# Kernel optimization log

Hardware: AMD Instinct MI355X
Metric: run time of the kernel (lower is better)

Reference implementation:

```python
import jax, jax.numpy as jnp
import numpy as np

N, OBS_LEN, PRED_LEN = 8192, 20, 30
EMBED, HIDDEN, CNN_OUT = 64, 128, 2048


def setup_inputs() -> dict:
    key = jax.random.key(0)
    ks = jax.random.split(key, 13)
    s = 0.05
    return {
        "img_embedding": jax.random.normal(ks[0], (N, CNN_OUT), jnp.float32),
        "obs_pos": jax.random.normal(ks[1], (N, OBS_LEN, 2), jnp.float32),
        "obs_hist_size": jax.random.randint(ks[2], (N,), 0, 20, jnp.int64) if jax.config.jax_enable_x64 else jax.random.randint(ks[2], (N,), 0, 20, jnp.int32),
        "obs_pos_rel": jax.random.normal(ks[3], (N, OBS_LEN, 2), jnp.float32),
        "h0": jax.random.normal(ks[4], (1, HIDDEN), jnp.float32) * s,
        "W_ih": jax.random.normal(ks[5], (4 * HIDDEN, EMBED), jnp.float32) * s,
        "W_hh": jax.random.normal(ks[6], (4 * HIDDEN, HIDDEN), jnp.float32) * s,
        "b_ih": jax.random.normal(ks[7], (4 * HIDDEN,), jnp.float32) * s,
        "b_hh": jax.random.normal(ks[8], (4 * HIDDEN,), jnp.float32) * s,
        "embed_W": jax.random.normal(ks[9], (EMBED, 2), jnp.float32) * s,
        "embed_b": jax.random.normal(ks[10], (EMBED,), jnp.float32) * s,
        "pred_W": jax.random.normal(ks[11], (2, HIDDEN + CNN_OUT), jnp.float32) * s,
        "pred_b": jax.random.normal(ks[12], (2,), jnp.float32) * s,
    }


def reference(img_embedding, obs_pos, obs_hist_size, obs_pos_rel,
              h0, W_ih, W_hh, b_ih, b_hh, embed_W, embed_b, pred_W, pred_b):
    n, obs_len = obs_pos.shape[0], obs_pos.shape[1]

    def lstm_cell(x_emb, h, c):
        # torch gate order: i, f, g, o
        gates = x_emb @ W_ih.T + b_ih + h @ W_hh.T + b_hh  # [n, 4H]
        i, f, g, o = jnp.split(gates, 4, axis=-1)
        c2 = jax.nn.sigmoid(f) * c + jax.nn.sigmoid(i) * jnp.tanh(g)
        h2 = jax.nn.sigmoid(o) * jnp.tanh(c2)
        return h2, c2

    def embed(rel):
        return jax.nn.relu(rel @ embed_W.T + embed_b)

    # NOTE: original code initializes BOTH h and c from h0 (faithful to source).
    h = jnp.broadcast_to(h0, (n, h0.shape[1]))
    c = h

    # ---- observation phase: t = 1 .. obs_len-1, masked update ----
    def obs_step(carry, inp):
        h, c = carry
        rel_t, t = inp
        mask = (obs_hist_size > (obs_len - t))[:, None]  # [n, 1]
        h2, c2 = lstm_cell(embed(rel_t), h, c)
        h = jnp.where(mask, h2, h)
        c = jnp.where(mask, c2, c)
        return (h, c), None

    ts = jnp.arange(1, obs_len)
    rel_seq = jnp.swapaxes(obs_pos_rel[:, 1:, :], 0, 1)  # [obs_len-1, n, 2]
    (h, c), _ = jax.lax.scan(obs_step, (h, c), (rel_seq, ts))

    def pred_step(carry, _):
        h, c, pos = carry
        disp = jnp.concatenate([h, img_embedding], axis=1) @ pred_W.T + pred_b  # [n, 2]
        pos = pos + disp
        h, c = lstm_cell(embed(disp), h, c)
        return (h, c, pos), pos

    pos0 = obs_pos[:, -1, :]
    _, traj = jax.lax.scan(pred_step, (h, c, pos0), None, length=PRED_LEN)
    return jnp.swapaxes(traj, 0, 1)  # [n, pred_len, 2]
```

## Files before the change

### kernel.cpp

```cpp
#include <hip/hip_runtime.h>

#define MBLK 32

typedef __attribute__((ext_vector_type(8))) short bf16x8;
typedef __attribute__((ext_vector_type(4))) short bf16x4;
typedef __attribute__((ext_vector_type(4))) float f32x4;

__device__ __forceinline__ unsigned short f2bf(float x){
  unsigned int u = __float_as_uint(x);
  u = u + 0x7FFFu + ((u >> 16) & 1u);
  return (unsigned short)(u >> 16);
}
__device__ __forceinline__ float bf2f(unsigned short s){
  return __uint_as_float(((unsigned int)s) << 16);
}
__device__ __forceinline__ float sigm(float x){
  return __builtin_amdgcn_rcpf(1.0f + __expf(-x));
}
__device__ __forceinline__ float tanh_(float x){
  return 1.0f - 2.0f*__builtin_amdgcn_rcpf(__expf(2.0f*x) + 1.0f);
}

__global__ __launch_bounds__(1024, 4) void traj_kernel(
    const float* __restrict__ img, const float* __restrict__ obs_pos,
    const int* __restrict__ hist, const float* __restrict__ rel,
    const float* __restrict__ h0, const float* __restrict__ W_ih,
    const float* __restrict__ W_hh, const float* __restrict__ b_ih,
    const float* __restrict__ b_hh, const float* __restrict__ eW,
    const float* __restrict__ eb, const float* __restrict__ pW,
    const float* __restrict__ pb, float* __restrict__ out)
{
  __shared__ unsigned short xh[2][MBLK*200];
  __shared__ float relL[MBLK*40];
  __shared__ float pwL[256];
  __shared__ float eW0[64], eW1[64], ebL[64];
  __shared__ float imgcL[MBLK*2];
  __shared__ float biasL[512];
  __shared__ float pbL[2];

  const int tid  = threadIdx.x;
  const int wv   = tid >> 6;
  const int lane = tid & 63;
  const int q    = lane >> 4;
  const int i    = lane & 15;
  const int par  = i & 1;
  const int j    = wv*8 + (i >> 1);
  const int g0   = blockIdx.x * MBLK;
  const int dm   = tid >> 5;
  const int i32  = tid & 31;

  for (int idx = tid; idx < MBLK*40; idx += 1024) relL[idx] = rel[g0*40 + idx];
  if (tid < 256) pwL[tid] = pW[(tid >> 7)*2176 + (tid & 127)];
  if (tid < 64){ eW0[tid] = eW[tid*2]; eW1[tid] = eW[tid*2+1]; ebL[tid] = eb[tid]; }
  if (tid < 512) biasL[tid] = b_ih[tid] + b_hh[tid];
  if (tid < 2) pbL[tid] = pb[tid];

  {
    const float* row = img + (size_t)(g0 + dm)*2048 + i32*64;
    const float* p0  = pW + 128 + i32*64;
    const float* p1  = pW + 2176 + 128 + i32*64;
    float s0 = 0.f, s1 = 0.f;
    #pragma unroll
    for (int v = 0; v < 16; v++){
      float4 a  = ((const float4*)row)[v];
      float4 w0 = ((const float4*)p0)[v];
      float4 w1 = ((const float4*)p1)[v];
      s0 += a.x*w0.x + a.y*w0.y + a.z*w0.z + a.w*w0.w;
      s1 += a.x*w1.x + a.y*w1.y + a.z*w1.z + a.w*w1.w;
    }
    #pragma unroll
    for (int msk = 1; msk < 32; msk <<= 1){
      s0 += __shfl_xor(s0, msk);
      s1 += __shfl_xor(s1, msk);
    }
    if (i32 == 0){ imgcL[dm*2] = s0; imgcL[dm*2+1] = s1; }
  }

  float h0j = h0[j];
  unsigned int thrpk = 0;
  float c_s[4];
  #pragma unroll
  for (int r = 0; r < 4; r++){
    int m = par*16 + q*4 + r;
    thrpk |= ((unsigned int)((20 - hist[g0 + m]) & 0xFF)) << (8*r);
    c_s[r] = h0j;
    xh[0][m*200 + 64 + j] = f2bf(h0j);
  }

  bf16x8 Bf[2][6];
  #pragma unroll
  for (int n2 = 0; n2 < 2; n2++){
    int row = (n2*2 + par)*128 + j;
    #pragma unroll
    for (int kt = 0; kt < 6; kt++){
      const float* src = (kt < 2) ? (W_ih + row*64  + kt*32      + q*8)
                                  : (W_hh + row*128 + (kt-2)*32  + q*8);
      float4 lo = ((const float4*)src)[0];
      float4 hi = ((const float4*)src)[1];
      bf16x8 tf;
      tf[0]=(short)f2bf(lo.x); tf[1]=(short)f2bf(lo.y); tf[2]=(short)f2bf(lo.z); tf[3]=(short)f2bf(lo.w);
      tf[4]=(short)f2bf(hi.x); tf[5]=(short)f2bf(hi.y); tf[6]=(short)f2bf(hi.z); tf[7]=(short)f2bf(hi.w);
      Bf[n2][kt] = tf;
    }
  }

  float pos_r = 0.f;
  if (i32 < 2) pos_r = obs_pos[(size_t)(g0 + dm)*40 + 38 + i32];

  __syncthreads();

  {
    int e0 = i32*2;
    float r0 = relL[dm*40 + 2], r1 = relL[dm*40 + 3];
    float a0 = fmaxf(0.f, r0*eW0[e0]   + r1*eW1[e0]   + ebL[e0]);
    float a1 = fmaxf(0.f, r0*eW0[e0+1] + r1*eW1[e0+1] + ebL[e0+1]);
    *((unsigned int*)&xh[0][dm*200 + e0]) =
        (unsigned int)f2bf(a0) | ((unsigned int)f2bf(a1) << 16);
  }

  int b = 0;

  for (int step = 0; step < 49; step++){
    const bool obs = (step < 19);
    __syncthreads();

    if (!obs){
      bf16x4 hv = *((const bf16x4*)&xh[b][dm*200 + 64 + i32*4]);
      float s0 = 0.f, s1 = 0.f;
      #pragma unroll
      for (int u = 0; u < 4; u++){
        float hf = bf2f((unsigned short)hv[u]);
        s0 += hf * pwL[i32*4 + u];
        s1 += hf * pwL[128 + i32*4 + u];
      }
      s0 += __shfl_xor(s0, 1);  s1 += __shfl_xor(s1, 1);
      s0 += __shfl_xor(s0, 2);  s1 += __shfl_xor(s1, 2);
      s0 += __shfl_xor(s0, 4);  s1 += __shfl_xor(s1, 4);
      s0 += __shfl_xor(s0, 8);  s1 += __shfl_xor(s1, 8);
      s0 += __shfl_xor(s0, 16); s1 += __shfl_xor(s1, 16);
      float d0 = s0 + imgcL[dm*2]   + pbL[0];
      float d1 = s1 + imgcL[dm*2+1] + pbL[1];
      if (i32 < 2){
        pos_r += (i32 == 0) ? d0 : d1;
        out[(size_t)(g0 + dm)*60 + (size_t)(step - 19)*2 + i32] = pos_r;
      }
      int e0 = i32*2;
      float a0 = fmaxf(0.f, d0*eW0[e0]   + d1*eW1[e0]   + ebL[e0]);
      float a1 = fmaxf(0.f, d0*eW0[e0+1] + d1*eW1[e0+1] + ebL[e0+1]);
      *((unsigned int*)&xh[b][dm*200 + e0]) =
          (unsigned int)f2bf(a0) | ((unsigned int)f2bf(a1) << 16);
      __syncthreads();
    }

    const float bv0 = biasL[(par    )*128 + j];
    const float bv1 = biasL[(2 + par)*128 + j];
    f32x4 a00 = (f32x4){bv0, bv0, bv0, bv0};
    f32x4 a01 = (f32x4){bv1, bv1, bv1, bv1};
    f32x4 a10 = a00;
    f32x4 a11 = a01;
    {
      bf16x8 A[6];
      #pragma unroll
      for (int kt = 0; kt < 6; kt++)
        A[kt] = *((const bf16x8*)&xh[b][i*200 + kt*32 + q*8]);
      #pragma unroll
      for (int kt = 0; kt < 6; kt++){
        a00 = __builtin_amdgcn_mfma_f32_16x16x32_bf16(A[kt], Bf[0][kt], a00, 0, 0, 0);
        a01 = __builtin_amdgcn_mfma_f32_16x16x32_bf16(A[kt], Bf[1][kt], a01, 0, 0, 0);
      }
    }
    {
      bf16x8 A[6];
      #pragma unroll
      for (int kt = 0; kt < 6; kt++)
        A[kt] = *((const bf16x8*)&xh[b][(16 + i)*200 + kt*32 + q*8]);
      #pragma unroll
      for (int kt = 0; kt < 6; kt++){
        a10 = __builtin_amdgcn_mfma_f32_16x16x32_bf16(A[kt], Bf[0][kt], a10, 0, 0, 0);
        a11 = __builtin_amdgcn_mfma_f32_16x16x32_bf16(A[kt], Bf[1][kt], a11, 0, 0, 0);
      }
    }

    if (obs && step < 18){
      int tt = step + 2;
      int e0 = i32*2;
      float r0 = relL[dm*40 + tt*2], r1 = relL[dm*40 + tt*2 + 1];
      float a0 = fmaxf(0.f, r0*eW0[e0]   + r1*eW1[e0]   + ebL[e0]);
      float a1 = fmaxf(0.f, r0*eW0[e0+1] + r1*eW1[e0+1] + ebL[e0+1]);
      *((unsigned int*)&xh[b^1][dm*200 + e0]) =
          (unsigned int)f2bf(a0) | ((unsigned int)f2bf(a1) << 16);
    }

    f32x4 self0 = par ? a10 : a00;
    f32x4 self1 = par ? a11 : a01;
    f32x4 send0 = par ? a00 : a10;
    f32x4 send1 = par ? a01 : a11;

    #pragma unroll
    for (int r = 0; r < 4; r++){
      float y0 = __shfl_xor(send0[r], 1);
      float y1 = __shfl_xor(send1[r], 1);
      float a0 = self0[r];
      float a1 = self1[r];
      float ig = par ? y0 : a0;
      float fg = par ? a0 : y0;
      float gg = par ? y1 : a1;
      float og = par ? a1 : y1;
      float c2 = sigm(fg)*c_s[r] + sigm(ig)*tanh_(gg);
      float h2 = sigm(og)*tanh_(c2);
      unsigned short h2b = f2bf(h2);
      int m = par*16 + q*4 + r;
      if (obs){
        int thr = (int)((thrpk >> (8*r)) & 0xFFu);
        if (step < thr){
          c2  = c_s[r];
          h2b = xh[b][m*200 + 64 + j];
        }
      }
      c_s[r] = c2;
      xh[b^1][m*200 + 64 + j] = h2b;
    }

    b ^= 1;
  }
}

extern "C" void kernel_launch(void* const* d_in, const int* in_sizes, int n_in,
                              void* d_out, int out_size, void* d_ws, size_t ws_size,
                              hipStream_t stream){
  const float* img     = (const float*)d_in[0];
  const float* obs_pos = (const float*)d_in[1];
  const int*   hist    = (const int*)d_in[2];
  const float* rel     = (const float*)d_in[3];
  const float* h0      = (const float*)d_in[4];
  const float* W_ih    = (const float*)d_in[5];
  const float* W_hh    = (const float*)d_in[6];
  const float* b_ih    = (const float*)d_in[7];
  const float* b_hh    = (const float*)d_in[8];
  const float* eW      = (const float*)d_in[9];
  const float* eb      = (const float*)d_in[10];
  const float* pW      = (const float*)d_in[11];
  const float* pb      = (const float*)d_in[12];
  float* out = (float*)d_out;
  hipLaunchKernelGGL(traj_kernel, dim3(8192/MBLK), dim3(1024), 0, stream,
                     img, obs_pos, hist, rel, h0, W_ih, W_hh, b_ih, b_hh,
                     eW, eb, pW, pb, out);
}
```

Measured before the change: 304.9 us.

## Keep small weights in registers and transpose h via shuffles for vector LDS stores

Moves the prediction weights, embed weights, biases and image contribution out of shared memory and into per-thread registers, so the loop no longer issues those LDS reads. The float-to-bf16 rounding now uses the packed v_cvt_pk_bf16_f32 instruction. The new h values are transposed across lanes with shuffles and byte permutes so each lane writes 4 bf16 values in one 8-byte LDS store instead of four 2-byte scattered stores. Masked rows keep the previous packed h in registers rather than reading it back from LDS. The cost is higher register pressure under a 1024-thread launch bound, plus extra shuffle instructions.

```diff
diff --git a/kernel.cpp b/kernel.cpp
--- a/kernel.cpp
+++ b/kernel.cpp
@@ -19,6 +19,11 @@
 }
 __device__ __forceinline__ float tanh_(float x){
   return 1.0f - 2.0f*__builtin_amdgcn_rcpf(__expf(2.0f*x) + 1.0f);
+}
+__device__ __forceinline__ unsigned int pk_bf16(float lo, float hi){
+  unsigned int r;
+  asm("v_cvt_pk_bf16_f32 %0, %1, %2" : "=v"(r) : "v"(lo), "v"(hi));
+  return r;
 }
 
 __global__ __launch_bounds__(1024, 4) void traj_kernel(
@@ -32,11 +37,7 @@
 {
   __shared__ unsigned short xh[2][MBLK*200];
   __shared__ float relL[MBLK*40];
-  __shared__ float pwL[256];
-  __shared__ float eW0[64], eW1[64], ebL[64];
   __shared__ float imgcL[MBLK*2];
-  __shared__ float biasL[512];
-  __shared__ float pbL[2];
 
   const int tid  = threadIdx.x;
   const int wv   = tid >> 6;
@@ -44,16 +45,19 @@
   const int q    = lane >> 4;
   const int i    = lane & 15;
   const int par  = i & 1;
-  const int j    = wv*8 + (i >> 1);
+  const int jj   = i >> 1;
+  const int j    = wv*8 + jj;
+  const int jj2  = jj >> 2;
   const int g0   = blockIdx.x * MBLK;
   const int dm   = tid >> 5;
   const int i32  = tid & 31;
 
+  const int m_post = par*16 + q*4 + (jj & 3);
+  const int hq     = wv*8 + jj2*4;
+  const int wofs   = m_post*200 + 64 + hq;
+  const unsigned int selA = (jj & 1) ? 0x03020706u : 0x05040100u;
+
   for (int idx = tid; idx < MBLK*40; idx += 1024) relL[idx] = rel[g0*40 + idx];
-  if (tid < 256) pwL[tid] = pW[(tid >> 7)*2176 + (tid & 127)];
-  if (tid < 64){ eW0[tid] = eW[tid*2]; eW1[tid] = eW[tid*2+1]; ebL[tid] = eb[tid]; }
-  if (tid < 512) biasL[tid] = b_ih[tid] + b_hh[tid];
-  if (tid < 2) pbL[tid] = pb[tid];
 
   {
     const float* row = img + (size_t)(g0 + dm)*2048 + i32*64;
@@ -75,6 +79,16 @@
     }
     if (i32 == 0){ imgcL[dm*2] = s0; imgcL[dm*2+1] = s1; }
   }
+
+  const float bv0 = b_ih[par*128 + j]       + b_hh[par*128 + j];
+  const float bv1 = b_ih[(2 + par)*128 + j] + b_hh[(2 + par)*128 + j];
+  const int   e0  = i32*2;
+  const float wA0 = eW[e0*2],     wB0 = eW[e0*2 + 1];
+  const float wA1 = eW[(e0+1)*2], wB1 = eW[(e0+1)*2 + 1];
+  const float be0 = eb[e0],       be1 = eb[e0+1];
+  const float pb0 = pb[0],        pb1 = pb[1];
+  float pwa0 = pW[i32*4+0], pwa1 = pW[i32*4+1], pwa2 = pW[i32*4+2], pwa3 = pW[i32*4+3];
+  float pwb0 = pW[2176+i32*4+0], pwb1 = pW[2176+i32*4+1], pwb2 = pW[2176+i32*4+2], pwb3 = pW[2176+i32*4+3];
 
   float h0j = h0[j];
   unsigned int thrpk = 0;
@@ -86,6 +100,9 @@
     c_s[r] = h0j;
     xh[0][m*200 + 64 + j] = f2bf(h0j);
   }
+  const int thr_post = 20 - hist[g0 + m_post];
+  unsigned int oldP0 = pk_bf16(h0[hq],   h0[hq+1]);
+  unsigned int oldP1 = pk_bf16(h0[hq+2], h0[hq+3]);
 
   bf16x8 Bf[2][6];
   #pragma unroll
@@ -109,13 +126,13 @@
 
   __syncthreads();
 
+  const float imgc0 = imgcL[dm*2], imgc1 = imgcL[dm*2+1];
+
   {
-    int e0 = i32*2;
-    float r0 = relL[dm*40 + 2], r1 = relL[dm*40 + 3];
-    float a0 = fmaxf(0.f, r0*eW0[e0]   + r1*eW1[e0]   + ebL[e0]);
-    float a1 = fmaxf(0.f, r0*eW0[e0+1] + r1*eW1[e0+1] + ebL[e0+1]);
-    *((unsigned int*)&xh[0][dm*200 + e0]) =
-        (unsigned int)f2bf(a0) | ((unsigned int)f2bf(a1) << 16);
+    float2 rr = *((const float2*)&relL[dm*40 + 2]);
+    float a0 = fmaxf(0.f, rr.x*wA0 + rr.y*wB0 + be0);
+    float a1 = fmaxf(0.f, rr.x*wA1 + rr.y*wB1 + be1);
+    *((unsigned int*)&xh[0][dm*200 + e0]) = pk_bf16(a0, a1);
   }
 
   int b = 0;
@@ -126,34 +143,29 @@
 
     if (!obs){
       bf16x4 hv = *((const bf16x4*)&xh[b][dm*200 + 64 + i32*4]);
-      float s0 = 0.f, s1 = 0.f;
-      #pragma unroll
-      for (int u = 0; u < 4; u++){
-        float hf = bf2f((unsigned short)hv[u]);
-        s0 += hf * pwL[i32*4 + u];
-        s1 += hf * pwL[128 + i32*4 + u];
-      }
+      float h0f = bf2f((unsigned short)hv[0]);
+      float h1f = bf2f((unsigned short)hv[1]);
+      float h2f_ = bf2f((unsigned short)hv[2]);
+      float h3f = bf2f((unsigned short)hv[3]);
+      float s0 = h0f*pwa0 + h1f*pwa1 + h2f_*pwa2 + h3f*pwa3;
+      float s1 = h0f*pwb0 + h1f*pwb1 + h2f_*pwb2 + h3f*pwb3;
       s0 += __shfl_xor(s0, 1);  s1 += __shfl_xor(s1, 1);
       s0 += __shfl_xor(s0, 2);  s1 += __shfl_xor(s1, 2);
       s0 += __shfl_xor(s0, 4);  s1 += __shfl_xor(s1, 4);
       s0 += __shfl_xor(s0, 8);  s1 += __shfl_xor(s1, 8);
       s0 += __shfl_xor(s0, 16); s1 += __shfl_xor(s1, 16);
-      float d0 = s0 + imgcL[dm*2]   + pbL[0];
-      float d1 = s1 + imgcL[dm*2+1] + pbL[1];
+      float d0 = s0 + imgc0 + pb0;
+      float d1 = s1 + imgc1 + pb1;
       if (i32 < 2){
         pos_r += (i32 == 0) ? d0 : d1;
         out[(size_t)(g0 + dm)*60 + (size_t)(step - 19)*2 + i32] = pos_r;
       }
-      int e0 = i32*2;
-      float a0 = fmaxf(0.f, d0*eW0[e0]   + d1*eW1[e0]   + ebL[e0]);
-      float a1 = fmaxf(0.f, d0*eW0[e0+1] + d1*eW1[e0+1] + ebL[e0+1]);
-      *((unsigned int*)&xh[b][dm*200 + e0]) =
-          (unsigned int)f2bf(a0) | ((unsigned int)f2bf(a1) << 16);
+      float a0 = fmaxf(0.f, d0*wA0 + d1*wB0 + be0);
+      float a1 = fmaxf(0.f, d0*wA1 + d1*wB1 + be1);
+      *((unsigned int*)&xh[b][dm*200 + e0]) = pk_bf16(a0, a1);
       __syncthreads();
     }
 
-    const float bv0 = biasL[(par    )*128 + j];
-    const float bv1 = biasL[(2 + par)*128 + j];
     f32x4 a00 = (f32x4){bv0, bv0, bv0, bv0};
     f32x4 a01 = (f32x4){bv1, bv1, bv1, bv1};
     f32x4 a10 = a00;
@@ -183,12 +195,10 @@
 
     if (obs && step < 18){
       int tt = step + 2;
-      int e0 = i32*2;
-      float r0 = relL[dm*40 + tt*2], r1 = relL[dm*40 + tt*2 + 1];
-      float a0 = fmaxf(0.f, r0*eW0[e0]   + r1*eW1[e0]   + ebL[e0]);
-      float a1 = fmaxf(0.f, r0*eW0[e0+1] + r1*eW1[e0+1] + ebL[e0+1]);
-      *((unsigned int*)&xh[b^1][dm*200 + e0]) =
-          (unsigned int)f2bf(a0) | ((unsigned int)f2bf(a1) << 16);
+      float2 rr = *((const float2*)&relL[dm*40 + tt*2]);
+      float a0 = fmaxf(0.f, rr.x*wA0 + rr.y*wB0 + be0);
+      float a1 = fmaxf(0.f, rr.x*wA1 + rr.y*wB1 + be1);
+      *((unsigned int*)&xh[b^1][dm*200 + e0]) = pk_bf16(a0, a1);
     }
 
     f32x4 self0 = par ? a10 : a00;
@@ -196,6 +206,7 @@
     f32x4 send0 = par ? a00 : a10;
     f32x4 send1 = par ? a01 : a11;
 
+    float h2f[4];
     #pragma unroll
     for (int r = 0; r < 4; r++){
       float y0 = __shfl_xor(send0[r], 1);
@@ -208,18 +219,31 @@
       float og = par ? a1 : y1;
       float c2 = sigm(fg)*c_s[r] + sigm(ig)*tanh_(gg);
       float h2 = sigm(og)*tanh_(c2);
-      unsigned short h2b = f2bf(h2);
-      int m = par*16 + q*4 + r;
       if (obs){
         int thr = (int)((thrpk >> (8*r)) & 0xFFu);
-        if (step < thr){
-          c2  = c_s[r];
-          h2b = xh[b][m*200 + 64 + j];
-        }
+        if (step < thr) c2 = c_s[r];
       }
       c_s[r] = c2;
-      xh[b^1][m*200 + 64 + j] = h2b;
-    }
+      h2f[r] = h2;
+    }
+
+    unsigned int P0 = pk_bf16(h2f[0], h2f[1]);
+    unsigned int P1 = pk_bf16(h2f[2], h2f[3]);
+    unsigned int X0 = __shfl_xor(P0, 2);
+    unsigned int X1 = __shfl_xor(P1, 2);
+    P0 = __builtin_amdgcn_perm(X0, P0, selA);
+    P1 = __builtin_amdgcn_perm(X1, P1, selA);
+    unsigned int Z0 = __shfl_xor(P0, 4);
+    unsigned int Z1 = __shfl_xor(P1, 4);
+    unsigned int Q0 = (jj & 2) ? Z1 : P0;
+    unsigned int Q1 = (jj & 2) ? P1 : Z0;
+    if (obs){
+      bool keep = (step < thr_post);
+      Q0 = keep ? oldP0 : Q0;
+      Q1 = keep ? oldP1 : Q1;
+      oldP0 = Q0; oldP1 = Q1;
+    }
+    *((uint2*)&xh[b^1][wofs]) = make_uint2(Q0, Q1);
 
     b ^= 1;
   }
```

After: 341.3 us. +12.0%, slower.
